# Optimization experiments

Hardware: AMD Instinct MI355X
Metric: run time of the kernel (lower is better)

## Reference

```python
import jax, jax.numpy as jnp
import numpy as np

B, T, N, D, C = 32, 256, 256, 1024, 80
SIM_THRESH = 0.7
MAX_AGE = 10
W_SIM, W_IOU = 0.7, 0.3


def setup_inputs() -> dict:
    key = jax.random.key(0)
    ks = jax.random.split(key, 8)
    track_memory = jax.random.normal(ks[0], (B, T, D), jnp.float32)
    track_boxes = jax.random.uniform(ks[1], (B, T, 4), jnp.float32, 0.05, 0.95)
    track_active = jax.random.bernoulli(ks[2], 0.9, (B, T))
    track_age = jax.random.randint(ks[3], (B, T), 0, 5, jnp.int32)
    track_hits = jax.random.randint(ks[4], (B, T), 1, 10, jnp.int32)
    det_boxes = jax.random.uniform(ks[5], (B, N, 4), jnp.float32, 0.05, 0.95)
    # correlate detections with tracks so cosine similarity exceeds the
    # matching threshold for many pairs and the greedy loop does real work
    det_memory = track_memory + 0.3 * jax.random.normal(ks[6], (B, N, D), jnp.float32)
    class_logits = jax.random.normal(ks[7], (B, N, C), jnp.float32)
    return {
        'track_memory': track_memory, 'track_boxes': track_boxes,
        'track_active': track_active, 'track_age': track_age,
        'track_hits': track_hits, 'det_boxes': det_boxes,
        'det_memory': det_memory, 'class_logits': class_logits,
    }


def _normalize(x):
    # matches F.normalize(dim=-1): x / max(||x||, eps)
    n = jnp.linalg.norm(x, axis=-1, keepdims=True)
    return x / jnp.maximum(n, 1e-12)


def _iou_matrix(tb, db):
    # tb [T,4], db [N,4], boxes in (cx, cy, w, h) format -> IoU [T,N]
    t_x1, t_y1 = tb[:, 0] - tb[:, 2] / 2, tb[:, 1] - tb[:, 3] / 2
    t_x2, t_y2 = tb[:, 0] + tb[:, 2] / 2, tb[:, 1] + tb[:, 3] / 2
    d_x1, d_y1 = db[:, 0] - db[:, 2] / 2, db[:, 1] - db[:, 3] / 2
    d_x2, d_y2 = db[:, 0] + db[:, 2] / 2, db[:, 1] + db[:, 3] / 2
    iw = jnp.clip(jnp.minimum(t_x2[:, None], d_x2[None, :]) - jnp.maximum(t_x1[:, None], d_x1[None, :]), 0.0)
    ih = jnp.clip(jnp.minimum(t_y2[:, None], d_y2[None, :]) - jnp.maximum(t_y1[:, None], d_y1[None, :]), 0.0)
    inter = iw * ih
    union = (tb[:, 2] * tb[:, 3])[:, None] + (db[:, 2] * db[:, 3])[None, :] - inter
    return inter / (union + 1e-6)


def _greedy_match(Cmat):
    # sequential greedy argmax matching, as in the torch while-loop.
    # returns match_det [T]: detection index matched to each track, -1 if none.
    Tn, Nn = Cmat.shape

    def step(carry, _):
        Cm, match_det = carry
        flat = Cm.reshape(-1)
        idx = jnp.argmax(flat)
        val = flat[idx]
        ok = val >= SIM_THRESH
        t = idx // Nn
        d = idx % Nn
        match_det = jnp.where(ok, match_det.at[t].set(d.astype(jnp.int32)), match_det)
        Cm = jnp.where(ok, Cm.at[t, :].set(-1.0).at[:, d].set(-1.0), Cm)
        return (Cm, match_det), None

    init = (Cmat, jnp.full((Tn,), -1, jnp.int32))
    (_, match_det), _ = jax.lax.scan(step, init, None, length=min(Tn, Nn))
    return match_det


def reference(track_memory, track_boxes, track_active, track_age, track_hits,
              det_boxes, det_memory, class_logits):
    # detection scores (computed in torch update(); not used downstream)
    scores = jnp.max(jax.nn.softmax(class_logits, axis=-1), axis=-1)  # [B,N]

    def per_batch(tm, tb, ta, age, hits, db, dm):
        sim = _normalize(tm) @ _normalize(dm).T            # [T,N] cosine sim
        iou = _iou_matrix(tb, db)                          # [T,N]
        Cmat = W_SIM * sim + W_IOU * iou
        Cmat = jnp.where(ta[:, None], Cmat, -1.0)          # inactive rows -> -1
        match_det = _greedy_match(Cmat)                    # [T]
        matched = match_det >= 0
        d = jnp.clip(match_det, 0)
        new_mem = jnp.where(matched[:, None], dm[d], tm)
        new_box = jnp.where(matched[:, None], db[d], tb)
        new_hits = jnp.where(matched, hits + 1, hits)
        unmatched_active = ta & ~matched
        new_age = jnp.where(matched, 0, jnp.where(unmatched_active, age + 1, age))
        new_active = jnp.where(matched, True,
                               jnp.where(unmatched_active, new_age <= MAX_AGE, ta))
        return new_mem, new_box, new_active, new_age, new_hits, match_det

    new_mem, new_box, new_active, new_age, new_hits, match_det = jax.vmap(per_batch)(
        track_memory, track_boxes, track_active, track_age, track_hits,
        det_boxes, det_memory)
    return new_mem, new_box, new_active, new_age, new_hits, match_det, scores
```

## Files before the change

kernel.cpp:

```cpp
#include <hip/hip_runtime.h>
#include <math.h>

static constexpr int PB = 32, PT = 256, PN = 256, PD = 1024, PC = 80;
static constexpr int BCAP = 96;
static constexpr int CAP  = 256;
static constexpr int NT   = 32;

static constexpr size_t O_MEM   = 0;
static constexpr size_t O_BOX   = O_MEM   + (size_t)PB*PT*PD;
static constexpr size_t O_ACT   = O_BOX   + (size_t)PB*PT*4;
static constexpr size_t O_AGE   = O_ACT   + (size_t)PB*PT;
static constexpr size_t O_HITS  = O_AGE   + (size_t)PB*PT;
static constexpr size_t O_MATCH = O_HITS  + (size_t)PB*PT;
static constexpr size_t O_SCORE = O_MATCH + (size_t)PB*PT;

typedef __attribute__((ext_vector_type(8))) short short8;
typedef __attribute__((ext_vector_type(4))) float f32x4;

__device__ __forceinline__ unsigned ordbits(float f) {
    unsigned b = __float_as_uint(f);
    return (b & 0x80000000u) ? ~b : (b | 0x80000000u);
}
__device__ __forceinline__ unsigned short f2bf(float f) {
    unsigned u = __float_as_uint(f);
    unsigned r = u + 0x7fffu + ((u >> 16) & 1u);
    return (unsigned short)(r >> 16);
}

__device__ __forceinline__ float box_cost(float sim, float4 bt, float4 bd) {
    float tX1 = bt.x - bt.z*0.5f, tX2 = bt.x + bt.z*0.5f;
    float tY1 = bt.y - bt.w*0.5f, tY2 = bt.y + bt.w*0.5f;
    float dX1 = bd.x - bd.z*0.5f, dX2 = bd.x + bd.z*0.5f;
    float dY1 = bd.y - bd.w*0.5f, dY2 = bd.y + bd.w*0.5f;
    float iw = fmaxf(fminf(tX2, dX2) - fmaxf(tX1, dX1), 0.f);
    float ih = fmaxf(fminf(tY2, dY2) - fmaxf(tY1, dY1), 0.f);
    float inter = iw * ih;
    float iou = inter / (bt.z*bt.w + bd.z*bd.w - inter + 1e-6f);
    return 0.7f * sim + 0.3f * iou;
}

__global__ __launch_bounds__(256) void k_cost(
        const float* __restrict__ tm, const float* __restrict__ dm,
        const float* __restrict__ tb, const float* __restrict__ db,
        const unsigned* __restrict__ ta,
        unsigned* __restrict__ cntblk, int* __restrict__ cand,
        float* __restrict__ asums, float* __restrict__ bsums,
        float* __restrict__ ddots) {
    __shared__ short As[32][40];
    __shared__ short Bs[64][40];
    __shared__ float ainv[32], binv[64];
    __shared__ unsigned bcnt;

    const int b = blockIdx.z;
    const int rowbase = blockIdx.y * 32;
    const int colbase = blockIdx.x * 64;
    const bool diag = ((blockIdx.y >> 1) == blockIdx.x);
    const bool odd  = (blockIdx.y & 1) != 0;
    const int bid = (b * 8 + blockIdx.y) * 4 + blockIdx.x;
    const int tid  = threadIdx.x;
    const int c    = tid & 7;
    const int r0   = tid >> 3;
    const int w    = tid >> 6;
    const int wm   = w >> 1, wn = w & 1;
    const int lane = tid & 63;
    const int m16  = lane & 15, quad = lane >> 4;

    if (tid == 0) bcnt = 0u;

    const float* Abase = tm + ((size_t)b * PT + rowbase) * PD;
    const float* Bbase = dm + ((size_t)b * PN + colbase) * PD;

    f32x4 acc[2];
    acc[0] = (f32x4)0.f; acc[1] = (f32x4)0.f;

    float asum = 0.f, bsum0 = 0.f, bsum1 = 0.f, dsum = 0.f;
    float4 av, bv0, bv1;

    av  = *(const float4*)(Abase + (size_t)r0 * PD + c * 4);
    bv0 = *(const float4*)(Bbase + (size_t)r0 * PD + c * 4);
    bv1 = *(const float4*)(Bbase + (size_t)(r0 + 32) * PD + c * 4);

    for (int k0 = 0; k0 < PD; k0 += 32) {
        __syncthreads();
        {
            float4 a = av, u0 = bv0, u1 = bv1;
            asum  += a.x*a.x + a.y*a.y + a.z*a.z + a.w*a.w;
            bsum0 += u0.x*u0.x + u0.y*u0.y + u0.z*u0.z + u0.w*u0.w;
            bsum1 += u1.x*u1.x + u1.y*u1.y + u1.z*u1.z + u1.w*u1.w;
            float4 d = odd ? u1 : u0;
            dsum  += a.x*d.x + a.y*d.y + a.z*d.z + a.w*d.w;
            uint2 pa, p0, p1;
            pa.x = f2bf(a.x)  | ((unsigned)f2bf(a.y)  << 16);
            pa.y = f2bf(a.z)  | ((unsigned)f2bf(a.w)  << 16);
            p0.x = f2bf(u0.x) | ((unsigned)f2bf(u0.y) << 16);
            p0.y = f2bf(u0.z) | ((unsigned)f2bf(u0.w) << 16);
            p1.x = f2bf(u1.x) | ((unsigned)f2bf(u1.y) << 16);
            p1.y = f2bf(u1.z) | ((unsigned)f2bf(u1.w) << 16);
            *(uint2*)&As[r0][c * 4]      = pa;
            *(uint2*)&Bs[r0][c * 4]      = p0;
            *(uint2*)&Bs[r0 + 32][c * 4] = p1;
        }
        __syncthreads();
        if (k0 + 32 < PD) {
            av  = *(const float4*)(Abase + (size_t)r0 * PD + k0 + 32 + c * 4);
            bv0 = *(const float4*)(Bbase + (size_t)r0 * PD + k0 + 32 + c * 4);
            bv1 = *(const float4*)(Bbase + (size_t)(r0 + 32) * PD + k0 + 32 + c * 4);
        }
        short8 af, bf[2];
        af = *(const short8*)&As[wm * 16 + m16][quad * 8];
#pragma unroll
        for (int nj = 0; nj < 2; ++nj)
            bf[nj] = *(const short8*)&Bs[wn * 32 + nj * 16 + m16][quad * 8];
#pragma unroll
        for (int nj = 0; nj < 2; ++nj)
            acc[nj] = __builtin_amdgcn_mfma_f32_16x16x32_bf16(
                af, bf[nj], acc[nj], 0, 0, 0);
    }

#pragma unroll
    for (int o = 1; o < 8; o <<= 1) {
        asum  += __shfl_xor(asum, o);
        bsum0 += __shfl_xor(bsum0, o);
        bsum1 += __shfl_xor(bsum1, o);
        dsum  += __shfl_xor(dsum, o);
    }
    __syncthreads();
    if (c == 0) {
        ainv[r0]      = 1.0f / fmaxf(sqrtf(asum), 1e-12f);
        binv[r0]      = 1.0f / fmaxf(sqrtf(bsum0), 1e-12f);
        binv[r0 + 32] = 1.0f / fmaxf(sqrtf(bsum1), 1e-12f);
        asums[b * PT + rowbase + r0] = asum;
        bsums[b * PN + colbase + r0]      = bsum0;
        bsums[b * PN + colbase + r0 + 32] = bsum1;
        if (diag) ddots[b * PT + rowbase + r0] = dsum;
    }
    __syncthreads();

    float dx1[2], dy1[2], dx2[2], dy2[2], darea[2], dnv[2];
    int ng[2];
#pragma unroll
    for (int nj = 0; nj < 2; ++nj) {
        int nl = wn * 32 + nj * 16 + m16;
        ng[nj] = colbase + nl;
        dnv[nj] = binv[nl];
        float4 bx = *(const float4*)&db[((size_t)b * PN + ng[nj]) * 4];
        dx1[nj] = bx.x - bx.z * 0.5f; dx2[nj] = bx.x + bx.z * 0.5f;
        dy1[nj] = bx.y - bx.w * 0.5f; dy2[nj] = bx.y + bx.w * 0.5f;
        darea[nj] = bx.z * bx.w;
    }

#pragma unroll
    for (int r = 0; r < 4; ++r) {
        int tl = wm * 16 + quad * 4 + r;
        int tg = rowbase + tl;
        if (ta[b * PT + tg] == 0u) continue;
        float tnv = ainv[tl];
        float4 bx = *(const float4*)&tb[((size_t)b * PT + tg) * 4];
        float tX1 = bx.x - bx.z * 0.5f, tX2 = bx.x + bx.z * 0.5f;
        float tY1 = bx.y - bx.w * 0.5f, tY2 = bx.y + bx.w * 0.5f;
        float tA = bx.z * bx.w;
#pragma unroll
        for (int nj = 0; nj < 2; ++nj) {
            float sim = acc[nj][r] * tnv * dnv[nj];
            float iw = fmaxf(fminf(tX2, dx2[nj]) - fmaxf(tX1, dx1[nj]), 0.f);
            float ih = fmaxf(fminf(tY2, dy2[nj]) - fmaxf(tY1, dy1[nj]), 0.f);
            float inter = iw * ih;
            float iou = inter / (tA + darea[nj] - inter + 1e-6f);
            float cost = 0.7f * sim + 0.3f * iou;
            if (cost >= 0.695f) {
                unsigned idx = atomicAdd(&bcnt, 1u);
                if (idx < BCAP) cand[bid * BCAP + idx] = (tg << 8) | ng[nj];
            }
        }
    }
    __syncthreads();
    if (tid == 0) cntblk[bid] = (bcnt > BCAP) ? BCAP : bcnt;
}

__global__ __launch_bounds__(256) void k_match(
        const float* __restrict__ tm, const float* __restrict__ dm,
        const float* __restrict__ tb, const float* __restrict__ db,
        const float* __restrict__ asums, const float* __restrict__ bsums,
        const float* __restrict__ ddots,
        const unsigned* __restrict__ cntblk, const int* __restrict__ cand,
        int* __restrict__ md) {
    const int b = blockIdx.x;
    const int tid = threadIdx.x;
    const int w = tid >> 6, lane = tid & 63;
    __shared__ int cnts[NT];
    __shared__ unsigned long long sel_key[CAP];
    __shared__ unsigned sel_cnt;
    __shared__ int odd_slot[64];
    __shared__ unsigned odd_cnt;
    __shared__ int rcnt[PT];
    __shared__ int ccnt[PN];
    __shared__ int conflict;

    if (tid == 0) { sel_cnt = 0u; odd_cnt = 0u; conflict = 0; }
    if (tid < NT) {
        int cj = (int)cntblk[b * NT + tid];
        cnts[tid] = (cj > BCAP) ? BCAP : cj;
    }
    rcnt[tid] = 0; ccnt[tid] = 0;
    md[b * PT + tid] = -1;
    __syncthreads();

    for (int u = tid; u < NT * BCAP; u += 256) {
        int j = u / BCAP, i = u - j * BCAP;
        if (i >= cnts[j]) continue;
        int gidx = (b * NT + j) * BCAP + i;
        int pair = cand[gidx];
        int t = pair >> 8, n = pair & 255;
        if (t == n) {
            float na  = asums[b * PT + t];
            float nb  = bsums[b * PN + n];
            float dot = ddots[b * PT + t];
            float sim = dot * (1.0f / fmaxf(sqrtf(na), 1e-12f))
                            * (1.0f / fmaxf(sqrtf(nb), 1e-12f));
            float4 bt = *(const float4*)&tb[((size_t)b * PT + t) * 4];
            float4 bd = *(const float4*)&db[((size_t)b * PN + n) * 4];
            float cost = box_cost(sim, bt, bd);
            if (cost >= 0.7f) {
                unsigned s = atomicAdd(&sel_cnt, 1u);
                if (s < CAP)
                    sel_key[s] = ((unsigned long long)ordbits(cost) << 16)
                               | (unsigned long long)(65535 - pair);
            }
        } else {
            unsigned oi = atomicAdd(&odd_cnt, 1u);
            if (oi < 64) odd_slot[oi] = gidx;
        }
    }
    __syncthreads();

    int nodd = (int)odd_cnt; if (nodd > 64) nodd = 64;
    for (int j = w; j < nodd; j += 4) {
        int pair = cand[odd_slot[j]];
        int t = pair >> 8, n = pair & 255;
        const float4* tr = (const float4*)(tm + ((size_t)b * PT + t) * PD);
        const float4* dr = (const float4*)(dm + ((size_t)b * PN + n) * PD);
        float dot = 0.f;
#pragma unroll
        for (int q = 0; q < 4; ++q) {
            float4 v = tr[lane + 64 * q];
            float4 u = dr[lane + 64 * q];
            dot += v.x*u.x + v.y*u.y + v.z*u.z + v.w*u.w;
        }
#pragma unroll
        for (int o = 1; o < 64; o <<= 1) dot += __shfl_xor(dot, o);
        if (lane == 0) {
            float na = asums[b * PT + t], nb = bsums[b * PN + n];
            float sim = dot * (1.0f / fmaxf(sqrtf(na), 1e-12f))
                            * (1.0f / fmaxf(sqrtf(nb), 1e-12f));
            float4 bt = *(const float4*)&tb[((size_t)b * PT + t) * 4];
            float4 bd = *(const float4*)&db[((size_t)b * PN + n) * 4];
            float cost = box_cost(sim, bt, bd);
            if (cost >= 0.7f) {
                unsigned s = atomicAdd(&sel_cnt, 1u);
                if (s < CAP)
                    sel_key[s] = ((unsigned long long)ordbits(cost) << 16)
                               | (unsigned long long)(65535 - pair);
            }
        }
    }
    __syncthreads();

    const unsigned ns = (sel_cnt > (unsigned)CAP) ? (unsigned)CAP : sel_cnt;
    for (unsigned s = tid; s < ns; s += 256) {
        int flat = 65535 - (int)(sel_key[s] & 0xFFFFull);
        if (atomicAdd(&rcnt[flat >> 8], 1) >= 1) conflict = 1;
        if (atomicAdd(&ccnt[flat & 255], 1) >= 1) conflict = 1;
    }
    __syncthreads();

    if (!conflict) {
        for (unsigned s = tid; s < ns; s += 256) {
            int flat = 65535 - (int)(sel_key[s] & 0xFFFFull);
            md[b * PT + (flat >> 8)] = flat & 255;
        }
        return;
    }

    if (w == 0) {
        unsigned long long k[4];
#pragma unroll
        for (int s = 0; s < 4; ++s) {
            unsigned idx = (unsigned)lane + 64u * s;
            k[s] = (idx < ns) ? sel_key[idx] : 0ull;
        }
        int mdv[4] = {-1, -1, -1, -1};
        for (int it = 0; it < PT; ++it) {
            unsigned long long m = k[0];
            if (k[1] > m) m = k[1];
            if (k[2] > m) m = k[2];
            if (k[3] > m) m = k[3];
#pragma unroll
            for (int o = 1; o < 64; o <<= 1) {
                unsigned long long s = __shfl_xor(m, o);
                if (s > m) m = s;
            }
            if (m == 0ull) break;
            int flat = 65535 - (int)(m & 0xFFFFull);
            int t = flat >> 8, d = flat & 255;
            if ((t & 63) == lane) mdv[t >> 6] = d;
#pragma unroll
            for (int s = 0; s < 4; ++s) {
                if (k[s]) {
                    int f2 = 65535 - (int)(k[s] & 0xFFFFull);
                    if ((f2 >> 8) == t || (f2 & 255) == d) k[s] = 0ull;
                }
            }
        }
#pragma unroll
        for (int s = 0; s < 4; ++s) md[b * PT + s * 64 + lane] = mdv[s];
    }
}

__global__ __launch_bounds__(256) void k_outsc(
        const float* __restrict__ tm, const float* __restrict__ tb,
        const unsigned* __restrict__ ta, const int* __restrict__ age,
        const int* __restrict__ hits, const float* __restrict__ db,
        const float* __restrict__ dm, const int* __restrict__ md,
        const float* __restrict__ lg, float* __restrict__ out) {
    int bx = blockIdx.x;
    if (bx < PB * PT) {
        int idx = bx;
        int b = idx >> 8;
        int m = md[idx];
        bool matched = m >= 0;
        int d = matched ? m : 0;
        const float4* src = (const float4*)(matched ? dm + ((size_t)b * PN + d) * PD
                                                    : tm + (size_t)idx * PD);
        float4* dst = (float4*)(out + O_MEM + (size_t)idx * PD);
        dst[threadIdx.x] = src[threadIdx.x];
        if (threadIdx.x < 4) {
            const float* sb = matched ? db + ((size_t)b * PN + d) * 4
                                      : tb + (size_t)idx * 4;
            out[O_BOX + (size_t)idx * 4 + threadIdx.x] = sb[threadIdx.x];
        }
        if (threadIdx.x == 0) {
            bool tact = ta[idx] != 0u;
            int hh = hits[idx], ag = age[idx];
            int nh = matched ? hh + 1 : hh;
            bool unm = tact && !matched;
            int na = matched ? 0 : (unm ? ag + 1 : ag);
            bool nact = matched ? true : (unm ? (na <= 10) : tact);
            out[O_ACT   + idx] = nact ? 1.0f : 0.0f;
            out[O_AGE   + idx] = (float)na;
            out[O_HITS  + idx] = (float)nh;
            out[O_MATCH + idx] = (float)m;
        }
    } else {
        int row  = (bx - PB * PT) * 4 + (threadIdx.x >> 6);
        int lane = threadIdx.x & 63;
        const float* p = lg + (size_t)row * PC;
        float x0 = p[lane];
        float x1 = (lane < PC - 64) ? p[64 + lane] : -INFINITY;
        float m = fmaxf(x0, x1);
#pragma unroll
        for (int o = 32; o > 0; o >>= 1) m = fmaxf(m, __shfl_down(m, o));
        m = __shfl(m, 0);
        float s = expf(x0 - m) + ((lane < PC - 64) ? expf(x1 - m) : 0.f);
#pragma unroll
        for (int o = 32; o > 0; o >>= 1) s += __shfl_down(s, o);
        if (lane == 0) out[O_SCORE + row] = 1.0f / s;
    }
}

extern "C" void kernel_launch(void* const* d_in, const int* in_sizes, int n_in,
                              void* d_out, int out_size, void* d_ws, size_t ws_size,
                              hipStream_t stream) {
    const float*    tm   = (const float*)d_in[0];
    const float*    tb   = (const float*)d_in[1];
    const unsigned* ta   = (const unsigned*)d_in[2];
    const int*      age  = (const int*)d_in[3];
    const int*      hits = (const int*)d_in[4];
    const float*    db   = (const float*)d_in[5];
    const float*    dm   = (const float*)d_in[6];
    const float*    lg   = (const float*)d_in[7];
    float* out = (float*)d_out;

    char* ws = (char*)d_ws;
    unsigned* cntblk = (unsigned*)ws;
    int* cand        = (int*)(ws + 4096);
    int* md          = (int*)(ws + 4096 + 393216);
    float* asums     = (float*)(ws + 4096 + 393216 + 32768);
    float* bsums     = asums + PB * PT;
    float* ddots     = bsums + PB * PN;

    k_cost <<<dim3(4, 8, PB), 256, 0, stream>>>(tm, dm, tb, db, ta,
                                                cntblk, cand, asums, bsums, ddots);
    k_match<<<dim3(PB), 256, 0, stream>>>(tm, dm, tb, db, asums, bsums, ddots,
                                          cntblk, cand, md);
    k_outsc<<<dim3(PB * PT + PB * PN / 4), 256, 0, stream>>>(
        tm, tb, ta, age, hits, db, dm, md, lg, out);
}
```

Measured before the change: 162.0 us.

## Split bf16 conversion into prep kernel and use 64x64 direct-load MFMA tiles

Adds a prep kernel that converts track and detection memory to bf16 once, computes row norms and diagonal dots, and also takes over the softmax score work that used to sit in the output kernel. The similarity kernel now reads the bf16 operands straight from global memory without staging through LDS, and each block covers a 64x64 tile with four MFMA accumulators per wave, so the candidate block count drops from 32 to 16 per batch. This removes the per-tile fp32 conversion and the LDS synchronisation from the GEMM loop. In exchange it adds an extra pass that writes and rereads 32 MB of bf16 data, plus one more kernel launch.

Result: slower. 170.2 us (+5.1%).

```diff
diff --git a/kernel.cpp b/kernel.cpp
--- a/kernel.cpp
+++ b/kernel.cpp
@@ -4,7 +4,7 @@
 static constexpr int PB = 32, PT = 256, PN = 256, PD = 1024, PC = 80;
 static constexpr int BCAP = 96;
 static constexpr int CAP  = 256;
-static constexpr int NT   = 32;
+static constexpr int NT   = 16;
 
 static constexpr size_t O_MEM   = 0;
 static constexpr size_t O_BOX   = O_MEM   + (size_t)PB*PT*PD;
@@ -39,110 +39,114 @@
     return 0.7f * sim + 0.3f * iou;
 }
 
-__global__ __launch_bounds__(256) void k_cost(
+__global__ __launch_bounds__(256) void k_prep(
         const float* __restrict__ tm, const float* __restrict__ dm,
+        const float* __restrict__ lg,
+        short* __restrict__ abf, short* __restrict__ bbf,
+        float* __restrict__ asums, float* __restrict__ bsums,
+        float* __restrict__ ddots, float* __restrict__ out) {
+    const int bx = blockIdx.x;
+    const int tid = threadIdx.x;
+    if (bx < PB * PT) {
+        const size_t row = (size_t)bx;
+        const float4 a = *(const float4*)(tm + row * PD + tid * 4);
+        const float4 d = *(const float4*)(dm + row * PD + tid * 4);
+        uint2 pa, pd2;
+        pa.x  = f2bf(a.x) | ((unsigned)f2bf(a.y) << 16);
+        pa.y  = f2bf(a.z) | ((unsigned)f2bf(a.w) << 16);
+        pd2.x = f2bf(d.x) | ((unsigned)f2bf(d.y) << 16);
+        pd2.y = f2bf(d.z) | ((unsigned)f2bf(d.w) << 16);
+        *(uint2*)(abf + row * PD + tid * 4) = pa;
+        *(uint2*)(bbf + row * PD + tid * 4) = pd2;
+        float as = a.x*a.x + a.y*a.y + a.z*a.z + a.w*a.w;
+        float bs = d.x*d.x + d.y*d.y + d.z*d.z + d.w*d.w;
+        float dd = a.x*d.x + a.y*d.y + a.z*d.z + a.w*d.w;
+#pragma unroll
+        for (int o = 1; o < 64; o <<= 1) {
+            as += __shfl_xor(as, o);
+            bs += __shfl_xor(bs, o);
+            dd += __shfl_xor(dd, o);
+        }
+        __shared__ float red[3][4];
+        const int w = tid >> 6, lane = tid & 63;
+        if (lane == 0) { red[0][w] = as; red[1][w] = bs; red[2][w] = dd; }
+        __syncthreads();
+        if (tid == 0) {
+            asums[row] = red[0][0] + red[0][1] + red[0][2] + red[0][3];
+            bsums[row] = red[1][0] + red[1][1] + red[1][2] + red[1][3];
+            ddots[row] = red[2][0] + red[2][1] + red[2][2] + red[2][3];
+        }
+    } else {
+        int rowi = (bx - PB * PT) * 4 + (tid >> 6);
+        int lane = tid & 63;
+        const float* p = lg + (size_t)rowi * PC;
+        float x0 = p[lane];
+        float x1 = (lane < PC - 64) ? p[64 + lane] : -INFINITY;
+        float m = fmaxf(x0, x1);
+#pragma unroll
+        for (int o = 32; o > 0; o >>= 1) m = fmaxf(m, __shfl_down(m, o));
+        m = __shfl(m, 0);
+        float s = expf(x0 - m) + ((lane < PC - 64) ? expf(x1 - m) : 0.f);
+#pragma unroll
+        for (int o = 32; o > 0; o >>= 1) s += __shfl_down(s, o);
+        if (lane == 0) out[O_SCORE + rowi] = 1.0f / s;
+    }
+}
+
+__global__ __launch_bounds__(256) void k_sim(
+        const short* __restrict__ abf, const short* __restrict__ bbf,
         const float* __restrict__ tb, const float* __restrict__ db,
         const unsigned* __restrict__ ta,
-        unsigned* __restrict__ cntblk, int* __restrict__ cand,
-        float* __restrict__ asums, float* __restrict__ bsums,
-        float* __restrict__ ddots) {
-    __shared__ short As[32][40];
-    __shared__ short Bs[64][40];
-    __shared__ float ainv[32], binv[64];
+        const float* __restrict__ asums, const float* __restrict__ bsums,
+        unsigned* __restrict__ cntblk, int* __restrict__ cand) {
+    const int b = blockIdx.z;
+    const int rowbase = blockIdx.y * 64;
+    const int colbase = blockIdx.x * 64;
+    const int bid = b * NT + blockIdx.y * 4 + blockIdx.x;
+    const int tid = threadIdx.x;
+    const int w = tid >> 6, lane = tid & 63;
+    const int wm = w >> 1, wn = w & 1;
+    const int m16 = lane & 15, quad = lane >> 4;
+
     __shared__ unsigned bcnt;
-
-    const int b = blockIdx.z;
-    const int rowbase = blockIdx.y * 32;
-    const int colbase = blockIdx.x * 64;
-    const bool diag = ((blockIdx.y >> 1) == blockIdx.x);
-    const bool odd  = (blockIdx.y & 1) != 0;
-    const int bid = (b * 8 + blockIdx.y) * 4 + blockIdx.x;
-    const int tid  = threadIdx.x;
-    const int c    = tid & 7;
-    const int r0   = tid >> 3;
-    const int w    = tid >> 6;
-    const int wm   = w >> 1, wn = w & 1;
-    const int lane = tid & 63;
-    const int m16  = lane & 15, quad = lane >> 4;
-
+    __shared__ float ainv[64], binv[64];
     if (tid == 0) bcnt = 0u;
-
-    const float* Abase = tm + ((size_t)b * PT + rowbase) * PD;
-    const float* Bbase = dm + ((size_t)b * PN + colbase) * PD;
-
-    f32x4 acc[2];
-    acc[0] = (f32x4)0.f; acc[1] = (f32x4)0.f;
-
-    float asum = 0.f, bsum0 = 0.f, bsum1 = 0.f, dsum = 0.f;
-    float4 av, bv0, bv1;
-
-    av  = *(const float4*)(Abase + (size_t)r0 * PD + c * 4);
-    bv0 = *(const float4*)(Bbase + (size_t)r0 * PD + c * 4);
-    bv1 = *(const float4*)(Bbase + (size_t)(r0 + 32) * PD + c * 4);
-
-    for (int k0 = 0; k0 < PD; k0 += 32) {
-        __syncthreads();
-        {
-            float4 a = av, u0 = bv0, u1 = bv1;
-            asum  += a.x*a.x + a.y*a.y + a.z*a.z + a.w*a.w;
-            bsum0 += u0.x*u0.x + u0.y*u0.y + u0.z*u0.z + u0.w*u0.w;
-            bsum1 += u1.x*u1.x + u1.y*u1.y + u1.z*u1.z + u1.w*u1.w;
-            float4 d = odd ? u1 : u0;
-            dsum  += a.x*d.x + a.y*d.y + a.z*d.z + a.w*d.w;
-            uint2 pa, p0, p1;
-            pa.x = f2bf(a.x)  | ((unsigned)f2bf(a.y)  << 16);
-            pa.y = f2bf(a.z)  | ((unsigned)f2bf(a.w)  << 16);
-            p0.x = f2bf(u0.x) | ((unsigned)f2bf(u0.y) << 16);
-            p0.y = f2bf(u0.z) | ((unsigned)f2bf(u0.w) << 16);
-            p1.x = f2bf(u1.x) | ((unsigned)f2bf(u1.y) << 16);
-            p1.y = f2bf(u1.z) | ((unsigned)f2bf(u1.w) << 16);
-            *(uint2*)&As[r0][c * 4]      = pa;
-            *(uint2*)&Bs[r0][c * 4]      = p0;
-            *(uint2*)&Bs[r0 + 32][c * 4] = p1;
-        }
-        __syncthreads();
-        if (k0 + 32 < PD) {
-            av  = *(const float4*)(Abase + (size_t)r0 * PD + k0 + 32 + c * 4);
-            bv0 = *(const float4*)(Bbase + (size_t)r0 * PD + k0 + 32 + c * 4);
-            bv1 = *(const float4*)(Bbase + (size_t)(r0 + 32) * PD + k0 + 32 + c * 4);
-        }
-        short8 af, bf[2];
-        af = *(const short8*)&As[wm * 16 + m16][quad * 8];
-#pragma unroll
-        for (int nj = 0; nj < 2; ++nj)
-            bf[nj] = *(const short8*)&Bs[wn * 32 + nj * 16 + m16][quad * 8];
-#pragma unroll
-        for (int nj = 0; nj < 2; ++nj)
-            acc[nj] = __builtin_amdgcn_mfma_f32_16x16x32_bf16(
-                af, bf[nj], acc[nj], 0, 0, 0);
-    }
-
-#pragma unroll
-    for (int o = 1; o < 8; o <<= 1) {
-        asum  += __shfl_xor(asum, o);
-        bsum0 += __shfl_xor(bsum0, o);
-        bsum1 += __shfl_xor(bsum1, o);
-        dsum  += __shfl_xor(dsum, o);
-    }
-    __syncthreads();
-    if (c == 0) {
-        ainv[r0]      = 1.0f / fmaxf(sqrtf(asum), 1e-12f);
-        binv[r0]      = 1.0f / fmaxf(sqrtf(bsum0), 1e-12f);
-        binv[r0 + 32] = 1.0f / fmaxf(sqrtf(bsum1), 1e-12f);
-        asums[b * PT + rowbase + r0] = asum;
-        bsums[b * PN + colbase + r0]      = bsum0;
-        bsums[b * PN + colbase + r0 + 32] = bsum1;
-        if (diag) ddots[b * PT + rowbase + r0] = dsum;
-    }
+    if (tid < 64)
+        ainv[tid] = 1.0f / fmaxf(sqrtf(asums[b * PT + rowbase + tid]), 1e-12f);
+    else if (tid < 128)
+        binv[tid - 64] = 1.0f / fmaxf(sqrtf(bsums[b * PN + colbase + tid - 64]), 1e-12f);
+
+    const short* Ab = abf + ((size_t)b * PT + rowbase) * PD;
+    const short* Bb = bbf + ((size_t)b * PN + colbase) * PD;
+    const short8* pA0 = (const short8*)(Ab + (size_t)(wm * 32 +      m16) * PD) + quad;
+    const short8* pA1 = (const short8*)(Ab + (size_t)(wm * 32 + 16 + m16) * PD) + quad;
+    const short8* pB0 = (const short8*)(Bb + (size_t)(wn * 32 +      m16) * PD) + quad;
+    const short8* pB1 = (const short8*)(Bb + (size_t)(wn * 32 + 16 + m16) * PD) + quad;
+
+    f32x4 acc00 = (f32x4)0.f, acc01 = (f32x4)0.f;
+    f32x4 acc10 = (f32x4)0.f, acc11 = (f32x4)0.f;
+#pragma unroll 8
+    for (int kk = 0; kk < PD / 32; ++kk) {
+        short8 a0 = pA0[kk * 4];
+        short8 a1 = pA1[kk * 4];
+        short8 b0 = pB0[kk * 4];
+        short8 b1 = pB1[kk * 4];
+        acc00 = __builtin_amdgcn_mfma_f32_16x16x32_bf16(a0, b0, acc00, 0, 0, 0);
+        acc01 = __builtin_amdgcn_mfma_f32_16x16x32_bf16(a0, b1, acc01, 0, 0, 0);
+        acc10 = __builtin_amdgcn_mfma_f32_16x16x32_bf16(a1, b0, acc10, 0, 0, 0);
+        acc11 = __builtin_amdgcn_mfma_f32_16x16x32_bf16(a1, b1, acc11, 0, 0, 0);
+    }
+    f32x4 accm[2][2] = {{acc00, acc01}, {acc10, acc11}};
+
     __syncthreads();
 
     float dx1[2], dy1[2], dx2[2], dy2[2], darea[2], dnv[2];
     int ng[2];
 #pragma unroll
     for (int nj = 0; nj < 2; ++nj) {
-        int nl = wn * 32 + nj * 16 + m16;
-        ng[nj] = colbase + nl;
-        dnv[nj] = binv[nl];
+        int cl = wn * 32 + nj * 16 + m16;
+        ng[nj] = colbase + cl;
+        dnv[nj] = binv[cl];
         float4 bx = *(const float4*)&db[((size_t)b * PN + ng[nj]) * 4];
         dx1[nj] = bx.x - bx.z * 0.5f; dx2[nj] = bx.x + bx.z * 0.5f;
         dy1[nj] = bx.y - bx.w * 0.5f; dy2[nj] = bx.y + bx.w * 0.5f;
@@ -150,26 +154,29 @@
     }
 
 #pragma unroll
-    for (int r = 0; r < 4; ++r) {
-        int tl = wm * 16 + quad * 4 + r;
-        int tg = rowbase + tl;
-        if (ta[b * PT + tg] == 0u) continue;
-        float tnv = ainv[tl];
-        float4 bx = *(const float4*)&tb[((size_t)b * PT + tg) * 4];
-        float tX1 = bx.x - bx.z * 0.5f, tX2 = bx.x + bx.z * 0.5f;
-        float tY1 = bx.y - bx.w * 0.5f, tY2 = bx.y + bx.w * 0.5f;
-        float tA = bx.z * bx.w;
-#pragma unroll
-        for (int nj = 0; nj < 2; ++nj) {
-            float sim = acc[nj][r] * tnv * dnv[nj];
-            float iw = fmaxf(fminf(tX2, dx2[nj]) - fmaxf(tX1, dx1[nj]), 0.f);
-            float ih = fmaxf(fminf(tY2, dy2[nj]) - fmaxf(tY1, dy1[nj]), 0.f);
-            float inter = iw * ih;
-            float iou = inter / (tA + darea[nj] - inter + 1e-6f);
-            float cost = 0.7f * sim + 0.3f * iou;
-            if (cost >= 0.695f) {
-                unsigned idx = atomicAdd(&bcnt, 1u);
-                if (idx < BCAP) cand[bid * BCAP + idx] = (tg << 8) | ng[nj];
+    for (int mi = 0; mi < 2; ++mi) {
+#pragma unroll
+        for (int r = 0; r < 4; ++r) {
+            int tl = wm * 32 + mi * 16 + quad * 4 + r;
+            int tg = rowbase + tl;
+            if (ta[b * PT + tg] == 0u) continue;
+            float tnv = ainv[tl];
+            float4 bx = *(const float4*)&tb[((size_t)b * PT + tg) * 4];
+            float tX1 = bx.x - bx.z * 0.5f, tX2 = bx.x + bx.z * 0.5f;
+            float tY1 = bx.y - bx.w * 0.5f, tY2 = bx.y + bx.w * 0.5f;
+            float tA = bx.z * bx.w;
+#pragma unroll
+            for (int nj = 0; nj < 2; ++nj) {
+                float sim = accm[mi][nj][r] * tnv * dnv[nj];
+                float iw = fmaxf(fminf(tX2, dx2[nj]) - fmaxf(tX1, dx1[nj]), 0.f);
+                float ih = fmaxf(fminf(tY2, dy2[nj]) - fmaxf(tY1, dy1[nj]), 0.f);
+                float inter = iw * ih;
+                float iou = inter / (tA + darea[nj] - inter + 1e-6f);
+                float cost = 0.7f * sim + 0.3f * iou;
+                if (cost >= 0.695f) {
+                    unsigned idx = atomicAdd(&bcnt, 1u);
+                    if (idx < BCAP) cand[bid * BCAP + idx] = (tg << 8) | ng[nj];
+                }
             }
         }
     }
@@ -321,49 +328,32 @@
         const unsigned* __restrict__ ta, const int* __restrict__ age,
         const int* __restrict__ hits, const float* __restrict__ db,
         const float* __restrict__ dm, const int* __restrict__ md,
-        const float* __restrict__ lg, float* __restrict__ out) {
-    int bx = blockIdx.x;
-    if (bx < PB * PT) {
-        int idx = bx;
-        int b = idx >> 8;
-        int m = md[idx];
-        bool matched = m >= 0;
-        int d = matched ? m : 0;
-        const float4* src = (const float4*)(matched ? dm + ((size_t)b * PN + d) * PD
-                                                    : tm + (size_t)idx * PD);
-        float4* dst = (float4*)(out + O_MEM + (size_t)idx * PD);
-        dst[threadIdx.x] = src[threadIdx.x];
-        if (threadIdx.x < 4) {
-            const float* sb = matched ? db + ((size_t)b * PN + d) * 4
-                                      : tb + (size_t)idx * 4;
-            out[O_BOX + (size_t)idx * 4 + threadIdx.x] = sb[threadIdx.x];
-        }
-        if (threadIdx.x == 0) {
-            bool tact = ta[idx] != 0u;
-            int hh = hits[idx], ag = age[idx];
-            int nh = matched ? hh + 1 : hh;
-            bool unm = tact && !matched;
-            int na = matched ? 0 : (unm ? ag + 1 : ag);
-            bool nact = matched ? true : (unm ? (na <= 10) : tact);
-            out[O_ACT   + idx] = nact ? 1.0f : 0.0f;
-            out[O_AGE   + idx] = (float)na;
-            out[O_HITS  + idx] = (float)nh;
-            out[O_MATCH + idx] = (float)m;
-        }
-    } else {
-        int row  = (bx - PB * PT) * 4 + (threadIdx.x >> 6);
-        int lane = threadIdx.x & 63;
-        const float* p = lg + (size_t)row * PC;
-        float x0 = p[lane];
-        float x1 = (lane < PC - 64) ? p[64 + lane] : -INFINITY;
-        float m = fmaxf(x0, x1);
-#pragma unroll
-        for (int o = 32; o > 0; o >>= 1) m = fmaxf(m, __shfl_down(m, o));
-        m = __shfl(m, 0);
-        float s = expf(x0 - m) + ((lane < PC - 64) ? expf(x1 - m) : 0.f);
-#pragma unroll
-        for (int o = 32; o > 0; o >>= 1) s += __shfl_down(s, o);
-        if (lane == 0) out[O_SCORE + row] = 1.0f / s;
+        float* __restrict__ out) {
+    int idx = blockIdx.x;
+    int b = idx >> 8;
+    int m = md[idx];
+    bool matched = m >= 0;
+    int d = matched ? m : 0;
+    const float4* src = (const float4*)(matched ? dm + ((size_t)b * PN + d) * PD
+                                                : tm + (size_t)idx * PD);
+    float4* dst = (float4*)(out + O_MEM + (size_t)idx * PD);
+    dst[threadIdx.x] = src[threadIdx.x];
+    if (threadIdx.x < 4) {
+        const float* sb = matched ? db + ((size_t)b * PN + d) * 4
+                                  : tb + (size_t)idx * 4;
+        out[O_BOX + (size_t)idx * 4 + threadIdx.x] = sb[threadIdx.x];
+    }
+    if (threadIdx.x == 0) {
+        bool tact = ta[idx] != 0u;
+        int hh = hits[idx], ag = age[idx];
+        int nh = matched ? hh + 1 : hh;
+        bool unm = tact && !matched;
+        int na = matched ? 0 : (unm ? ag + 1 : ag);
+        bool nact = matched ? true : (unm ? (na <= 10) : tact);
+        out[O_ACT   + idx] = nact ? 1.0f : 0.0f;
+        out[O_AGE   + idx] = (float)na;
+        out[O_HITS  + idx] = (float)nh;
+        out[O_MATCH + idx] = (float)m;
     }
 }
 
@@ -381,17 +371,21 @@
     float* out = (float*)d_out;
 
     char* ws = (char*)d_ws;
-    unsigned* cntblk = (unsigned*)ws;
-    int* cand        = (int*)(ws + 4096);
-    int* md          = (int*)(ws + 4096 + 393216);
-    float* asums     = (float*)(ws + 4096 + 393216 + 32768);
-    float* bsums     = asums + PB * PT;
-    float* ddots     = bsums + PB * PN;
-
-    k_cost <<<dim3(4, 8, PB), 256, 0, stream>>>(tm, dm, tb, db, ta,
-                                                cntblk, cand, asums, bsums, ddots);
-    k_match<<<dim3(PB), 256, 0, stream>>>(tm, dm, tb, db, asums, bsums, ddots,
-                                          cntblk, cand, md);
-    k_outsc<<<dim3(PB * PT + PB * PN / 4), 256, 0, stream>>>(
-        tm, tb, ta, age, hits, db, dm, md, lg, out);
-}
+    short* abf   = (short*)ws;
+    short* bbf   = abf + (size_t)PB * PT * PD;
+    float* asums = (float*)(bbf + (size_t)PB * PN * PD);
+    float* bsums = asums + PB * PT;
+    float* ddots = bsums + PB * PN;
+    unsigned* cntblk = (unsigned*)(ddots + PB * PT);
+    int* cand = (int*)(cntblk + PB * NT);
+    int* md   = cand + PB * NT * BCAP;
+
+    k_prep <<<PB * PT + PB * PN / 4, 256, 0, stream>>>(
+        tm, dm, lg, abf, bbf, asums, bsums, ddots, out);
+    k_sim  <<<dim3(4, 4, PB), 256, 0, stream>>>(
+        abf, bbf, tb, db, ta, asums, bsums, cntblk, cand);
+    k_match<<<dim3(PB), 256, 0, stream>>>(
+        tm, dm, tb, db, asums, bsums, ddots, cntblk, cand, md);
+    k_outsc<<<dim3(PB * PT), 256, 0, stream>>>(
+        tm, tb, ta, age, hits, db, dm, md, out);
+}
```
